# Kernel optimization log

Hardware: AMD Instinct MI355X
Metric: run time of the kernel (lower is better)

Reference implementation:

```python
import jax, jax.numpy as jnp
import numpy as np

NUM_ITERS = 2      # num_iters default
NEG_SLOPE = 0.2    # LeakyReLU slope in GAT attention
NEG_INF = -1e9

N, E, B, H, K, L = 204800, 6144000, 4096, 8, 30, 50


def setup_inputs() -> dict:
    key = jax.random.key(0)
    ks = jax.random.split(key, 14)
    return {
        "target_features": jax.random.normal(ks[0], (N, 8), jnp.float32),
        "feature_dist_graph": jax.random.normal(ks[1], (E, 8), jnp.float32),
        "rij_dist_pairs": jax.random.uniform(ks[2], (E,), jnp.float32),
        "b_scope": jax.random.randint(ks[3], (N, K), 0, E + 1, jnp.int32),
        "start_end_env": jax.random.randint(ks[4], (N, K), 0, N + 1, jnp.int32),
        "l_scope": jax.random.randint(ks[5], (B, L), 0, N + 1, jnp.int32),
        "edge_src": jax.random.randint(ks[6], (E,), 0, N + 1, jnp.int32),
        "W_emb": jax.random.normal(ks[7], (8, H), jnp.float32),
        "b_emb": jax.random.normal(ks[8], (H,), jnp.float32),
        "W_dist": jax.random.normal(ks[9], (9, H), jnp.float32),
        "b_dist": jax.random.normal(ks[10], (H,), jnp.float32),
        "W_gat": jax.random.normal(ks[11], (H, H), jnp.float32),
        "a_src": jax.random.normal(ks[12], (H,), jnp.float32),
        "a_dst": jax.random.normal(ks[13], (H,), jnp.float32),
    }


def reference(target_features, feature_dist_graph, rij_dist_pairs,
              b_scope, start_end_env, l_scope, edge_src,
              W_emb, b_emb, W_dist, b_dist, W_gat, a_src, a_dst):
    # node embedding: [N, 8] -> [N, H]
    h = target_features @ W_emb + b_emb
    # edge (feature+distance) embedding: [E, 9] -> [E, H]
    msg = jnp.concatenate([feature_dist_graph, rij_dist_pairs[:, None]], axis=1) @ W_dist + b_dist
    zero = jnp.zeros((1, h.shape[1]), h.dtype)
    h = jnp.concatenate([zero, h], axis=0)          # zero row for 1-based / padded indices
    pad_mask = b_scope > 0                           # padded neighbor slots point at row 0
    for _ in range(NUM_ITERS):
        nbr_self = h[start_end_env]                  # getConnectedFeatures: [N, K, H] (target repeated)
        msg0 = jnp.concatenate([zero, msg], axis=0)  # zero row for padded edge indices
        nbr_msg = msg0[b_scope]                      # gathered neighbor messages [N, K, H]
        # GAT attention over the K neighbor slots
        z_s = nbr_self @ W_gat                       # [N, K, H]
        z_m = nbr_msg @ W_gat                        # [N, K, H]
        e = jax.nn.leaky_relu(z_s @ a_src + z_m @ a_dst, NEG_SLOPE)  # [N, K]
        e = jnp.where(pad_mask, e, NEG_INF)
        alpha = jax.nn.softmax(e, axis=1)            # [N, K]
        out = jnp.einsum('nk,nkh->nh', alpha, z_m)   # attention-weighted aggregate [N, H]
        h = jnp.concatenate([zero, jax.nn.elu(out)], axis=0)  # [N+1, H]
        # updateConnectedDict: scatter node states back to per-edge messages
        msg = h[edge_src]                            # [E, H]
    # readout: gather per-graph feature rows and sum -> mol_vecs [B, H]
    return h[l_scope].sum(axis=1)
```

## Files before the change

### kernel.cpp

```cpp
#include <hip/hip_runtime.h>

typedef float f32x4 __attribute__((ext_vector_type(4)));

#define NEG_SLOPE 0.2f
#define NEG_INF   -1e9f

__global__ void prep_embed(const float* __restrict__ fdg,
                           const float* __restrict__ rij,
                           const int* __restrict__ edge_src,
                           const float* __restrict__ W_dist,
                           const float* __restrict__ b_dist,
                           const float* __restrict__ W_gat,
                           const float* __restrict__ a_src,
                           const float* __restrict__ a_dst,
                           const float* __restrict__ tf,
                           const float* __restrict__ W_emb,
                           const float* __restrict__ b_emb,
                           float* __restrict__ rec,
                           float* __restrict__ h_a,
                           float* __restrict__ h_b,
                           float* __restrict__ t0,
                           float* __restrict__ t1,
                           int E, int N, int nb_edge) {
    __shared__ float sW[72];
    __shared__ float sb[8];
    __shared__ float sWg[64];
    __shared__ float s_vec[8];
    int tid = threadIdx.x;
    bool edge_block = (blockIdx.x < nb_edge);
    if (edge_block) {
        if (tid < 72) sW[tid] = W_dist[tid];
        else if (tid < 80) sb[tid - 72] = b_dist[tid - 72];
    } else {
        if (tid < 64) sW[tid] = W_emb[tid];
        else if (tid < 72) sb[tid - 64] = b_emb[tid - 64];
    }
    if (tid >= 128 && tid < 192) sWg[tid - 128] = W_gat[tid - 128];
    __syncthreads();
    if (tid < 8) {
        const float* av = edge_block ? a_dst : a_src;
        float s = 0.f;
        #pragma unroll
        for (int j = 0; j < 8; ++j) s += sWg[tid * 8 + j] * av[j];
        s_vec[tid] = s;
    }
    __syncthreads();

    if (edge_block) {
        int e = blockIdx.x * blockDim.x + tid;
        if (e >= E) return;
        const f32x4* fr = reinterpret_cast<const f32x4*>(fdg + (size_t)e * 8);
        f32x4 g0 = fr[0], g1 = fr[1];
        float rv = rij[e];
        float msg[8];
        #pragma unroll
        for (int j = 0; j < 8; ++j) {
            float s = sb[j];
            #pragma unroll
            for (int i = 0; i < 4; ++i) s += g0[i] * sW[i * 8 + j];
            #pragma unroll
            for (int i = 0; i < 4; ++i) s += g1[i] * sW[(4 + i) * 8 + j];
            s += rv * sW[64 + j];
            msg[j] = s;
        }
        float em = 0.f;
        #pragma unroll
        for (int j = 0; j < 8; ++j) em += msg[j] * s_vec[j];
        int src = edge_src[e];

        f32x4* op = reinterpret_cast<f32x4*>(rec + (size_t)e * 16);
        f32x4 m0 = {msg[0], msg[1], msg[2], msg[3]};
        f32x4 m1 = {msg[4], msg[5], msg[6], msg[7]};
        f32x4 m2 = {em, __int_as_float(src), 0.f, 0.f};
        op[0] = m0; op[1] = m1; op[2] = m2;
    } else {
        int n = (blockIdx.x - nb_edge) * blockDim.x + tid;
        if (n >= N) return;
        if (n == 0) {
            #pragma unroll
            for (int j = 0; j < 8; ++j) { h_a[j] = 0.f; h_b[j] = 0.f; }
            t0[0] = 0.f;
            t1[0] = 0.f;
        }
        const f32x4* tfr = reinterpret_cast<const f32x4*>(tf + (size_t)n * 8);
        f32x4 a = tfr[0], b = tfr[1];
        float x[8] = {a[0], a[1], a[2], a[3], b[0], b[1], b[2], b[3]};
        float out[8];
        #pragma unroll
        for (int j = 0; j < 8; ++j) out[j] = sb[j];
        #pragma unroll
        for (int i = 0; i < 8; ++i)
            #pragma unroll
            for (int j = 0; j < 8; ++j)
                out[j] += x[i] * sW[i * 8 + j];
        float t = 0.f;
        #pragma unroll
        for (int p = 0; p < 8; ++p) t += out[p] * s_vec[p];
        t0[n + 1] = t;
        f32x4* hr = reinterpret_cast<f32x4*>(h_a + (size_t)(n + 1) * 8);
        f32x4 o0 = {out[0], out[1], out[2], out[3]};
        f32x4 o1 = {out[4], out[5], out[6], out[7]};
        hr[0] = o0;
        hr[1] = o1;
    }
}

__device__ __forceinline__ void finish_node(const float msg[8], float t_se, float em,
                                            bool has, bool vk, int lane, int node,
                                            const float* __restrict__ sWg,
                                            const float* __restrict__ s_as,
                                            float* __restrict__ h_next,
                                            float* __restrict__ t_next) {
    float ee = t_se + em;
    ee = (ee >= 0.f) ? ee : NEG_SLOPE * ee;
    float e = has ? ee : (vk ? NEG_INF : -3e38f);

    float m = e;
    #pragma unroll
    for (int off = 16; off; off >>= 1) m = fmaxf(m, __shfl_xor(m, off, 32));
    float p = vk ? expf(e - m) : 0.f;
    float denom = p;
    #pragma unroll
    for (int off = 16; off; off >>= 1) denom += __shfl_xor(denom, off, 32);
    float alpha = p / denom;

    float agg[8];
    #pragma unroll
    for (int j = 0; j < 8; ++j) agg[j] = alpha * msg[j];
    #pragma unroll
    for (int off = 16; off; off >>= 1)
        #pragma unroll
        for (int j = 0; j < 8; ++j) agg[j] += __shfl_xor(agg[j], off, 32);

    if (lane < 8) {
        float o = 0.f;
        #pragma unroll
        for (int i = 0; i < 8; ++i) o += agg[i] * sWg[i * 8 + lane];
        o = (o > 0.f) ? o : (expf(o) - 1.f);
        h_next[(size_t)(node + 1) * 8 + lane] = o;
        if (t_next) {
            float tv = o * s_as[lane];
            tv += __shfl_xor(tv, 1, 32);
            tv += __shfl_xor(tv, 2, 32);
            tv += __shfl_xor(tv, 4, 32);
            if (lane == 0) t_next[node + 1] = tv;
        }
    }
}

__global__ void gat_iter1_rec(const float* __restrict__ t0,
                              float* __restrict__ h1,
                              float* __restrict__ t1,
                              int* __restrict__ src_idx,
                              const int* __restrict__ b_scope,
                              const int* __restrict__ se_env,
                              const float* __restrict__ rec,
                              const float* __restrict__ W_gat,
                              const float* __restrict__ a_src,
                              int N, int K) {
    __shared__ float sWg[64];
    __shared__ float s_as[8];
    int tid = threadIdx.x;
    if (tid < 64) sWg[tid] = W_gat[tid];
    __syncthreads();
    if (tid < 8) {
        float s = 0.f;
        #pragma unroll
        for (int j = 0; j < 8; ++j) s += sWg[tid * 8 + j] * a_src[j];
        s_as[tid] = s;
    }
    __syncthreads();

    int lane = tid & 31;
    int g = blockIdx.x * 8 + (tid >> 5);
    int nA = g * 2, nB = g * 2 + 1;
    if (nA >= N) return;
    bool hasBn = (nB < N);
    bool vk = (lane < K);

    int bsA = 0, seA = 0, bsB = 0, seB = 0;
    if (vk) {
        bsA = b_scope[(size_t)nA * K + lane];
        seA = se_env[(size_t)nA * K + lane];
        if (hasBn) {
            bsB = b_scope[(size_t)nB * K + lane];
            seB = se_env[(size_t)nB * K + lane];
        }
    }
    bool hasA = vk && (bsA > 0);
    bool hasB = vk && hasBn && (bsB > 0);

    float tA = vk ? t0[seA] : 0.f;
    float tB = (vk && hasBn) ? t0[seB] : 0.f;

    f32x4 a0 = {0,0,0,0}, a1 = {0,0,0,0}, a2 = {0,0,0,0};
    f32x4 b0 = {0,0,0,0}, b1 = {0,0,0,0}, b2 = {0,0,0,0};
    if (hasA) {
        const f32x4* rp = reinterpret_cast<const f32x4*>(rec + (size_t)(bsA - 1) * 16);
        a0 = rp[0]; a1 = rp[1]; a2 = rp[2];
    }
    if (hasB) {
        const f32x4* rp = reinterpret_cast<const f32x4*>(rec + (size_t)(bsB - 1) * 16);
        b0 = rp[0]; b1 = rp[1]; b2 = rp[2];
    }

    int srcA = hasA ? __float_as_int(a2[1]) : -1;
    int srcB = hasB ? __float_as_int(b2[1]) : -1;
    if (vk) {
        src_idx[(size_t)nA * K + lane] = srcA;
        if (hasBn) src_idx[(size_t)nB * K + lane] = srcB;
    }

    float msgA[8] = {a0[0], a0[1], a0[2], a0[3], a1[0], a1[1], a1[2], a1[3]};
    finish_node(msgA, tA, a2[0], hasA, vk, lane, nA, sWg, s_as, h1, t1);
    if (hasBn) {
        float msgB[8] = {b0[0], b0[1], b0[2], b0[3], b1[0], b1[1], b1[2], b1[3]};
        finish_node(msgB, tB, b2[0], hasB, vk, lane, nB, sWg, s_as, h1, t1);
    }
}

__global__ void gat_iter1_fb(const float* __restrict__ t0,
                             float* __restrict__ h1,
                             float* __restrict__ t1,
                             int* __restrict__ src_idx,
                             const int* __restrict__ b_scope,
                             const int* __restrict__ se_env,
                             const float* __restrict__ fdg,
                             const float* __restrict__ rij,
                             const int* __restrict__ edge_src,
                             const float* __restrict__ W_dist,
                             const float* __restrict__ b_dist,
                             const float* __restrict__ W_gat,
                             const float* __restrict__ a_src,
                             const float* __restrict__ a_dst,
                             int N, int K) {
    __shared__ float sWg[64];
    __shared__ float s_as[8];
    __shared__ float s_ad[8];
    __shared__ float sWd[72];
    __shared__ float sbd[8];
    int tid = threadIdx.x;
    if (tid < 64) sWg[tid] = W_gat[tid];
    if (tid >= 64 && tid < 136) sWd[tid - 64] = W_dist[tid - 64];
    if (tid >= 136 && tid < 144) sbd[tid - 136] = b_dist[tid - 136];
    __syncthreads();
    if (tid < 8) {
        float s = 0.f;
        #pragma unroll
        for (int j = 0; j < 8; ++j) s += sWg[tid * 8 + j] * a_src[j];
        s_as[tid] = s;
    } else if (tid < 16) {
        int i = tid - 8;
        float s = 0.f;
        #pragma unroll
        for (int j = 0; j < 8; ++j) s += sWg[i * 8 + j] * a_dst[j];
        s_ad[i] = s;
    }
    __syncthreads();

    int node = blockIdx.x * 8 + (tid >> 5);
    int lane = tid & 31;
    if (node >= N) return;
    bool vk = (lane < K);

    int bs = 0, se = 0;
    if (vk) {
        bs = b_scope[(size_t)node * K + lane];
        se = se_env[(size_t)node * K + lane];
    }
    bool has = vk && (bs > 0);
    float t_se = vk ? t0[se] : 0.f;

    float msg[8];
    #pragma unroll
    for (int j = 0; j < 8; ++j) msg[j] = 0.f;
    float em = 0.f;
    int src = -1;
    if (has) {
        const f32x4* fr = reinterpret_cast<const f32x4*>(fdg + (size_t)(bs - 1) * 8);
        f32x4 g0 = fr[0], g1 = fr[1];
        float rv = rij[bs - 1];
        src = edge_src[bs - 1];
        #pragma unroll
        for (int j = 0; j < 8; ++j) {
            float s = sbd[j];
            #pragma unroll
            for (int i = 0; i < 4; ++i) s += g0[i] * sWd[i * 8 + j];
            #pragma unroll
            for (int i = 0; i < 4; ++i) s += g1[i] * sWd[(4 + i) * 8 + j];
            s += rv * sWd[64 + j];
            msg[j] = s;
        }
        #pragma unroll
        for (int j = 0; j < 8; ++j) em += msg[j] * s_ad[j];
    }
    if (vk) src_idx[(size_t)node * K + lane] = src;
    finish_node(msg, t_se, em, has, vk, lane, node, sWg, s_as, h1, t1);
}

__global__ void gat_iter2(const float* __restrict__ h1,
                          const float* __restrict__ t1,
                          float* __restrict__ h2,
                          const int* __restrict__ src_idx,
                          const int* __restrict__ se_env,
                          const float* __restrict__ W_gat,
                          const float* __restrict__ a_dst,
                          int N, int K) {
    __shared__ float sWg[64];
    __shared__ float s_ad[8];
    int tid = threadIdx.x;
    if (tid < 64) sWg[tid] = W_gat[tid];
    __syncthreads();
    if (tid < 8) {
        float s = 0.f;
        #pragma unroll
        for (int j = 0; j < 8; ++j) s += sWg[tid * 8 + j] * a_dst[j];
        s_ad[tid] = s;
    }
    __syncthreads();

    int lane = tid & 31;
    int g = blockIdx.x * 8 + (tid >> 5);
    int nA = g * 2, nB = g * 2 + 1;
    if (nA >= N) return;
    bool hasBn = (nB < N);
    bool vk = (lane < K);

    int srcA = -1, seA = 0, srcB = -1, seB = 0;
    if (vk) {
        srcA = src_idx[(size_t)nA * K + lane];
        seA  = se_env[(size_t)nA * K + lane];
        if (hasBn) {
            srcB = src_idx[(size_t)nB * K + lane];
            seB  = se_env[(size_t)nB * K + lane];
        }
    }
    bool hasA = vk && (srcA >= 0);
    bool hasB = vk && hasBn && (srcB >= 0);

    float tA = vk ? t1[seA] : 0.f;
    float tB = (vk && hasBn) ? t1[seB] : 0.f;

    f32x4 a0 = {0,0,0,0}, a1 = {0,0,0,0}, b0 = {0,0,0,0}, b1 = {0,0,0,0};
    if (hasA) {
        const f32x4* mr = reinterpret_cast<const f32x4*>(h1 + (size_t)srcA * 8);
        a0 = mr[0]; a1 = mr[1];
    }
    if (hasB) {
        const f32x4* mr = reinterpret_cast<const f32x4*>(h1 + (size_t)srcB * 8);
        b0 = mr[0]; b1 = mr[1];
    }

    float msgA[8] = {a0[0], a0[1], a0[2], a0[3], a1[0], a1[1], a1[2], a1[3]};
    float emA = 0.f;
    #pragma unroll
    for (int j = 0; j < 8; ++j) emA += msgA[j] * s_ad[j];
    finish_node(msgA, tA, emA, hasA, vk, lane, nA, sWg, nullptr, h2, nullptr);
    if (hasBn) {
        float msgB[8] = {b0[0], b0[1], b0[2], b0[3], b1[0], b1[1], b1[2], b1[3]};
        float emB = 0.f;
        #pragma unroll
        for (int j = 0; j < 8; ++j) emB += msgB[j] * s_ad[j];
        finish_node(msgB, tB, emB, hasB, vk, lane, nB, sWg, nullptr, h2, nullptr);
    }
}

__global__ void readout_kernel(const float* __restrict__ h,
                               const int* __restrict__ l_scope,
                               float* __restrict__ out, int B, int L) {
    int gid = blockIdx.x * blockDim.x + threadIdx.x;
    int b = gid >> 3;
    int j = gid & 7;
    if (b >= B) return;
    float s = 0.f;
    for (int l = 0; l < L; ++l) {
        int idx = l_scope[(size_t)b * L + l];
        s += h[(size_t)idx * 8 + j];
    }
    out[(size_t)b * 8 + j] = s;
}

extern "C" void kernel_launch(void* const* d_in, const int* in_sizes, int n_in,
                              void* d_out, int out_size, void* d_ws, size_t ws_size,
                              hipStream_t stream) {
    const float* tf      = (const float*)d_in[0];
    const float* fdg     = (const float*)d_in[1];
    const float* rij     = (const float*)d_in[2];
    const int* b_scope   = (const int*)d_in[3];
    const int* start_env = (const int*)d_in[4];
    const int* l_scope   = (const int*)d_in[5];
    const int* edge_src  = (const int*)d_in[6];
    const float* W_emb   = (const float*)d_in[7];
    const float* b_emb   = (const float*)d_in[8];
    const float* W_dist  = (const float*)d_in[9];
    const float* b_dist  = (const float*)d_in[10];
    const float* W_gat   = (const float*)d_in[11];
    const float* a_src   = (const float*)d_in[12];
    const float* a_dst   = (const float*)d_in[13];
    float* out = (float*)d_out;

    const int N = in_sizes[0] / 8;
    const int E = in_sizes[1] / 8;
    const int K = in_sizes[3] / N;
    const int L = 50;
    const int B = in_sizes[5] / L;

    size_t rec_f = (size_t)E * 16;
    size_t need  = (rec_f + 2 * (size_t)(N + 1) * 8 + 2 * (size_t)(N + 1)
                    + (size_t)N * K) * 4;
    bool use_rec = (ws_size >= need);

    float* base = (float*)d_ws;
    float* rec  = base;
    size_t off  = use_rec ? rec_f : 0;
    float* h_a  = base + off;  off += (size_t)(N + 1) * 8;
    float* h_b  = base + off;  off += (size_t)(N + 1) * 8;
    float* t0v  = base + off;  off += (size_t)(N + 1);
    float* t1v  = base + off;  off += (size_t)(N + 1);
    int* src_idx = (int*)(base + off);

    const int nb_edge = (E + 255) / 256;
    const int nb_node = (N + 255) / 256;

    if (use_rec) {
        prep_embed<<<nb_edge + nb_node, 256, 0, stream>>>(
            fdg, rij, edge_src, W_dist, b_dist, W_gat, a_src, a_dst,
            tf, W_emb, b_emb, rec, h_a, h_b, t0v, t1v, E, N, nb_edge);
        const int g1_blocks = ((N + 1) / 2 + 7) / 8;
        gat_iter1_rec<<<g1_blocks, 256, 0, stream>>>(t0v, h_b, t1v, src_idx,
                                                     b_scope, start_env, rec,
                                                     W_gat, a_src, N, K);
    } else {
        prep_embed<<<nb_node, 256, 0, stream>>>(
            fdg, rij, edge_src, W_dist, b_dist, W_gat, a_src, a_dst,
            tf, W_emb, b_emb, rec, h_a, h_b, t0v, t1v, 0, N, 0);
        gat_iter1_fb<<<(N + 7) / 8, 256, 0, stream>>>(t0v, h_b, t1v, src_idx,
                                                      b_scope, start_env,
                                                      fdg, rij, edge_src,
                                                      W_dist, b_dist, W_gat,
                                                      a_src, a_dst, N, K);
    }

    const int g2_blocks = ((N + 1) / 2 + 7) / 8;
    gat_iter2<<<g2_blocks, 256, 0, stream>>>(h_b, t1v, h_a, src_idx, start_env,
                                             W_gat, a_dst, N, K);

    readout_kernel<<<(B * 8 + 255) / 256, 256, 0, stream>>>(h_a, l_scope, out, B, L);
}
```

Measured before the change: 458.9 us.

## Shrink edge record to 8 floats and drop src_idx buffer

The per-edge record written in prep_embed shrinks from 16 floats (message, precomputed attention term, source index) to the 8 message floats. The attention dot product now runs in gat_iter1_rec, which also goes back to one node per warp. The intermediate src_idx array is removed, and gat_iter2 instead reads b_scope and does an extra dependent gather through edge_src. This cuts write and read traffic on the large E-sized record, at the cost of an extra indirect load in the second iteration.

```diff
diff --git a/kernel.cpp b/kernel.cpp
--- a/kernel.cpp
+++ b/kernel.cpp
@@ -7,12 +7,10 @@
 
 __global__ void prep_embed(const float* __restrict__ fdg,
                            const float* __restrict__ rij,
-                           const int* __restrict__ edge_src,
                            const float* __restrict__ W_dist,
                            const float* __restrict__ b_dist,
                            const float* __restrict__ W_gat,
                            const float* __restrict__ a_src,
-                           const float* __restrict__ a_dst,
                            const float* __restrict__ tf,
                            const float* __restrict__ W_emb,
                            const float* __restrict__ b_emb,
@@ -34,14 +32,13 @@
     } else {
         if (tid < 64) sW[tid] = W_emb[tid];
         else if (tid < 72) sb[tid - 64] = b_emb[tid - 64];
-    }
-    if (tid >= 128 && tid < 192) sWg[tid - 128] = W_gat[tid - 128];
-    __syncthreads();
-    if (tid < 8) {
-        const float* av = edge_block ? a_dst : a_src;
-        float s = 0.f;
-        #pragma unroll
-        for (int j = 0; j < 8; ++j) s += sWg[tid * 8 + j] * av[j];
+        if (tid >= 128 && tid < 192) sWg[tid - 128] = W_gat[tid - 128];
+    }
+    __syncthreads();
+    if (!edge_block && tid < 8) {
+        float s = 0.f;
+        #pragma unroll
+        for (int j = 0; j < 8; ++j) s += sWg[tid * 8 + j] * a_src[j];
         s_vec[tid] = s;
     }
     __syncthreads();
@@ -63,16 +60,10 @@
             s += rv * sW[64 + j];
             msg[j] = s;
         }
-        float em = 0.f;
-        #pragma unroll
-        for (int j = 0; j < 8; ++j) em += msg[j] * s_vec[j];
-        int src = edge_src[e];
-
-        f32x4* op = reinterpret_cast<f32x4*>(rec + (size_t)e * 16);
+        f32x4* op = reinterpret_cast<f32x4*>(rec + (size_t)e * 8);
         f32x4 m0 = {msg[0], msg[1], msg[2], msg[3]};
         f32x4 m1 = {msg[4], msg[5], msg[6], msg[7]};
-        f32x4 m2 = {em, __int_as_float(src), 0.f, 0.f};
-        op[0] = m0; op[1] = m1; op[2] = m2;
+        op[0] = m0; op[1] = m1;
     } else {
         int n = (blockIdx.x - nb_edge) * blockDim.x + tid;
         if (n >= N) return;
@@ -151,15 +142,16 @@
 __global__ void gat_iter1_rec(const float* __restrict__ t0,
                               float* __restrict__ h1,
                               float* __restrict__ t1,
-                              int* __restrict__ src_idx,
                               const int* __restrict__ b_scope,
                               const int* __restrict__ se_env,
                               const float* __restrict__ rec,
                               const float* __restrict__ W_gat,
                               const float* __restrict__ a_src,
+                              const float* __restrict__ a_dst,
                               int N, int K) {
     __shared__ float sWg[64];
     __shared__ float s_as[8];
+    __shared__ float s_ad[8];
     int tid = threadIdx.x;
     if (tid < 64) sWg[tid] = W_gat[tid];
     __syncthreads();
@@ -168,66 +160,48 @@
         #pragma unroll
         for (int j = 0; j < 8; ++j) s += sWg[tid * 8 + j] * a_src[j];
         s_as[tid] = s;
-    }
-    __syncthreads();
-
+    } else if (tid < 16) {
+        int i = tid - 8;
+        float s = 0.f;
+        #pragma unroll
+        for (int j = 0; j < 8; ++j) s += sWg[i * 8 + j] * a_dst[j];
+        s_ad[i] = s;
+    }
+    __syncthreads();
+
+    int node = blockIdx.x * 8 + (tid >> 5);
     int lane = tid & 31;
-    int g = blockIdx.x * 8 + (tid >> 5);
-    int nA = g * 2, nB = g * 2 + 1;
-    if (nA >= N) return;
-    bool hasBn = (nB < N);
+    if (node >= N) return;
     bool vk = (lane < K);
 
-    int bsA = 0, seA = 0, bsB = 0, seB = 0;
+    int bs = 0, se = 0;
     if (vk) {
-        bsA = b_scope[(size_t)nA * K + lane];
-        seA = se_env[(size_t)nA * K + lane];
-        if (hasBn) {
-            bsB = b_scope[(size_t)nB * K + lane];
-            seB = se_env[(size_t)nB * K + lane];
-        }
-    }
-    bool hasA = vk && (bsA > 0);
-    bool hasB = vk && hasBn && (bsB > 0);
-
-    float tA = vk ? t0[seA] : 0.f;
-    float tB = (vk && hasBn) ? t0[seB] : 0.f;
-
-    f32x4 a0 = {0,0,0,0}, a1 = {0,0,0,0}, a2 = {0,0,0,0};
-    f32x4 b0 = {0,0,0,0}, b1 = {0,0,0,0}, b2 = {0,0,0,0};
-    if (hasA) {
-        const f32x4* rp = reinterpret_cast<const f32x4*>(rec + (size_t)(bsA - 1) * 16);
-        a0 = rp[0]; a1 = rp[1]; a2 = rp[2];
-    }
-    if (hasB) {
-        const f32x4* rp = reinterpret_cast<const f32x4*>(rec + (size_t)(bsB - 1) * 16);
-        b0 = rp[0]; b1 = rp[1]; b2 = rp[2];
-    }
-
-    int srcA = hasA ? __float_as_int(a2[1]) : -1;
-    int srcB = hasB ? __float_as_int(b2[1]) : -1;
-    if (vk) {
-        src_idx[(size_t)nA * K + lane] = srcA;
-        if (hasBn) src_idx[(size_t)nB * K + lane] = srcB;
-    }
-
-    float msgA[8] = {a0[0], a0[1], a0[2], a0[3], a1[0], a1[1], a1[2], a1[3]};
-    finish_node(msgA, tA, a2[0], hasA, vk, lane, nA, sWg, s_as, h1, t1);
-    if (hasBn) {
-        float msgB[8] = {b0[0], b0[1], b0[2], b0[3], b1[0], b1[1], b1[2], b1[3]};
-        finish_node(msgB, tB, b2[0], hasB, vk, lane, nB, sWg, s_as, h1, t1);
-    }
+        bs = b_scope[(size_t)node * K + lane];
+        se = se_env[(size_t)node * K + lane];
+    }
+    bool has = vk && (bs > 0);
+    float t_se = vk ? t0[se] : 0.f;
+
+    f32x4 m0 = {0,0,0,0}, m1 = {0,0,0,0};
+    if (has) {
+        const f32x4* rp = reinterpret_cast<const f32x4*>(rec + (size_t)(bs - 1) * 8);
+        m0 = rp[0]; m1 = rp[1];
+    }
+    float msg[8] = {m0[0], m0[1], m0[2], m0[3], m1[0], m1[1], m1[2], m1[3]};
+    float em = 0.f;
+    #pragma unroll
+    for (int j = 0; j < 8; ++j) em += msg[j] * s_ad[j];
+
+    finish_node(msg, t_se, em, has, vk, lane, node, sWg, s_as, h1, t1);
 }
 
 __global__ void gat_iter1_fb(const float* __restrict__ t0,
                              float* __restrict__ h1,
                              float* __restrict__ t1,
-                             int* __restrict__ src_idx,
                              const int* __restrict__ b_scope,
                              const int* __restrict__ se_env,
                              const float* __restrict__ fdg,
                              const float* __restrict__ rij,
-                             const int* __restrict__ edge_src,
                              const float* __restrict__ W_dist,
                              const float* __restrict__ b_dist,
                              const float* __restrict__ W_gat,
@@ -275,12 +249,10 @@
     #pragma unroll
     for (int j = 0; j < 8; ++j) msg[j] = 0.f;
     float em = 0.f;
-    int src = -1;
     if (has) {
         const f32x4* fr = reinterpret_cast<const f32x4*>(fdg + (size_t)(bs - 1) * 8);
         f32x4 g0 = fr[0], g1 = fr[1];
         float rv = rij[bs - 1];
-        src = edge_src[bs - 1];
         #pragma unroll
         for (int j = 0; j < 8; ++j) {
             float s = sbd[j];
@@ -294,15 +266,15 @@
         #pragma unroll
         for (int j = 0; j < 8; ++j) em += msg[j] * s_ad[j];
     }
-    if (vk) src_idx[(size_t)node * K + lane] = src;
     finish_node(msg, t_se, em, has, vk, lane, node, sWg, s_as, h1, t1);
 }
 
 __global__ void gat_iter2(const float* __restrict__ h1,
                           const float* __restrict__ t1,
                           float* __restrict__ h2,
-                          const int* __restrict__ src_idx,
+                          const int* __restrict__ b_scope,
                           const int* __restrict__ se_env,
+                          const int* __restrict__ edge_src,
                           const float* __restrict__ W_gat,
                           const float* __restrict__ a_dst,
                           int N, int K) {
@@ -326,20 +298,24 @@
     bool hasBn = (nB < N);
     bool vk = (lane < K);
 
-    int srcA = -1, seA = 0, srcB = -1, seB = 0;
+    int bsA = 0, seA = 0, bsB = 0, seB = 0;
     if (vk) {
-        srcA = src_idx[(size_t)nA * K + lane];
-        seA  = se_env[(size_t)nA * K + lane];
+        bsA = b_scope[(size_t)nA * K + lane];
+        seA = se_env[(size_t)nA * K + lane];
         if (hasBn) {
-            srcB = src_idx[(size_t)nB * K + lane];
-            seB  = se_env[(size_t)nB * K + lane];
+            bsB = b_scope[(size_t)nB * K + lane];
+            seB = se_env[(size_t)nB * K + lane];
         }
     }
-    bool hasA = vk && (srcA >= 0);
-    bool hasB = vk && hasBn && (srcB >= 0);
+    bool hasA = vk && (bsA > 0);
+    bool hasB = vk && hasBn && (bsB > 0);
 
     float tA = vk ? t1[seA] : 0.f;
     float tB = (vk && hasBn) ? t1[seB] : 0.f;
+
+    int srcA = 0, srcB = 0;
+    if (hasA) srcA = edge_src[bsA - 1];
+    if (hasB) srcB = edge_src[bsB - 1];
 
     f32x4 a0 = {0,0,0,0}, a1 = {0,0,0,0}, b0 = {0,0,0,0}, b1 = {0,0,0,0};
     if (hasA) {
@@ -405,9 +381,8 @@
     const int L = 50;
     const int B = in_sizes[5] / L;
 
-    size_t rec_f = (size_t)E * 16;
-    size_t need  = (rec_f + 2 * (size_t)(N + 1) * 8 + 2 * (size_t)(N + 1)
-                    + (size_t)N * K) * 4;
+    size_t rec_f = (size_t)E * 8;
+    size_t need  = (rec_f + 2 * (size_t)(N + 1) * 8 + 2 * (size_t)(N + 1)) * 4;
     bool use_rec = (ws_size >= need);
 
     float* base = (float*)d_ws;
@@ -416,34 +391,32 @@
     float* h_a  = base + off;  off += (size_t)(N + 1) * 8;
     float* h_b  = base + off;  off += (size_t)(N + 1) * 8;
     float* t0v  = base + off;  off += (size_t)(N + 1);
-    float* t1v  = base + off;  off += (size_t)(N + 1);
-    int* src_idx = (int*)(base + off);
+    float* t1v  = base + off;
 
     const int nb_edge = (E + 255) / 256;
     const int nb_node = (N + 255) / 256;
 
     if (use_rec) {
         prep_embed<<<nb_edge + nb_node, 256, 0, stream>>>(
-            fdg, rij, edge_src, W_dist, b_dist, W_gat, a_src, a_dst,
+            fdg, rij, W_dist, b_dist, W_gat, a_src,
             tf, W_emb, b_emb, rec, h_a, h_b, t0v, t1v, E, N, nb_edge);
-        const int g1_blocks = ((N + 1) / 2 + 7) / 8;
-        gat_iter1_rec<<<g1_blocks, 256, 0, stream>>>(t0v, h_b, t1v, src_idx,
-                                                     b_scope, start_env, rec,
-                                                     W_gat, a_src, N, K);
+        gat_iter1_rec<<<(N + 7) / 8, 256, 0, stream>>>(t0v, h_b, t1v,
+                                                       b_scope, start_env, rec,
+                                                       W_gat, a_src, a_dst, N, K);
     } else {
         prep_embed<<<nb_node, 256, 0, stream>>>(
-            fdg, rij, edge_src, W_dist, b_dist, W_gat, a_src, a_dst,
+            fdg, rij, W_dist, b_dist, W_gat, a_src,
             tf, W_emb, b_emb, rec, h_a, h_b, t0v, t1v, 0, N, 0);
-        gat_iter1_fb<<<(N + 7) / 8, 256, 0, stream>>>(t0v, h_b, t1v, src_idx,
+        gat_iter1_fb<<<(N + 7) / 8, 256, 0, stream>>>(t0v, h_b, t1v,
                                                       b_scope, start_env,
-                                                      fdg, rij, edge_src,
+                                                      fdg, rij,
                                                       W_dist, b_dist, W_gat,
                                                       a_src, a_dst, N, K);
     }
 
     const int g2_blocks = ((N + 1) / 2 + 7) / 8;
-    gat_iter2<<<g2_blocks, 256, 0, stream>>>(h_b, t1v, h_a, src_idx, start_env,
-                                             W_gat, a_dst, N, K);
+    gat_iter2<<<g2_blocks, 256, 0, stream>>>(h_b, t1v, h_a, b_scope, start_env,
+                                             edge_src, W_gat, a_dst, N, K);
 
     readout_kernel<<<(B * 8 + 255) / 256, 256, 0, stream>>>(h_a, l_scope, out, B, L);
 }
```

New measurement: 432.1 us. 5.8% less time.
